# Kernel optimization log

Measured on AMD Instinct MI355X. Metric: run time of the kernel, lower is better.

## Reference

```python
import jax, jax.numpy as jnp
import numpy as np
import math

HAD_BLOCK = 1024


def fwht(x):
    """Fast Walsh-Hadamard transform along the last axis (size must be power of 2)."""
    orig_shape = x.shape
    n = orig_shape[-1]
    x = x.reshape(-1, n)
    h = 1
    while h < n:  # log2(n) stages; static Python loop, jit-friendly
        x = x.reshape(-1, n // (2 * h), 2, h)
        a = x[:, :, 0, :]
        b = x[:, :, 1, :]
        x = jnp.stack([a + b, a - b], axis=2).reshape(-1, n)
        h *= 2
    return x.reshape(orig_shape)


def setup_inputs() -> dict:
    key = jax.random.key(0)
    kx, kw = jax.random.split(key)
    B, S, D_in, D_out = 4, 4096, 4096, 4096
    x = jax.random.normal(kx, (B, S, D_in), dtype=jnp.float32)
    # nn.Parameter(weight / sqrt(had_block_size)) in __init__
    weight = jax.random.normal(kw, (D_out, D_in), dtype=jnp.float32) / math.sqrt(HAD_BLOCK)
    return {"x": x, "weight": weight}


def reference(x, weight):
    n = x.shape[-1]
    padded = ((n - 1) // HAD_BLOCK + 1) * HAD_BLOCK
    if padded != n:
        pad_width = [(0, 0)] * (x.ndim - 1) + [(0, padded - n)]
        x = jnp.pad(x, pad_width)
    mult = padded // HAD_BLOCK
    xb = x.reshape(x.shape[:-1] + (mult, HAD_BLOCK))
    xb = fwht(xb) * (1.0 / math.sqrt(HAD_BLOCK))
    xh = xb.reshape(x.shape[:-1] + (mult * HAD_BLOCK,))
    # F.linear: x @ weight.T
    return jnp.einsum('bsi,oi->bso', xh, weight)
```

## Files before the change

### kernel.cpp

```cpp
#include <hip/hip_runtime.h>
#include <hip/hip_bf16.h>
#include <stdint.h>


typedef __attribute__((ext_vector_type(8))) short    short8;
typedef __attribute__((ext_vector_type(4))) float    f32x4;
typedef __attribute__((ext_vector_type(8))) uint16_t u16x8;

static constexpr int MDIM = 16384;
static constexpr int NDIM = 4096;
static constexpr int KDIM = 4096;
static constexpr int BM = 256, BN = 256, BK = 64;
static constexpr int NT = KDIM / BK;

__device__ __forceinline__ uint16_t f2bf(float f) {
  union { float f; uint32_t u; } c; c.f = f;
  uint32_t u = c.u;
  return (uint16_t)((u + 0x7FFFu + ((u >> 16) & 1u)) >> 16);
}

__global__ __launch_bounds__(256) void cvt_x_kernel(const float* __restrict__ x,
                                                    uint16_t* __restrict__ xb, int n8) {
  int stride = gridDim.x * blockDim.x;
  for (int t = blockIdx.x * blockDim.x + threadIdx.x; t < n8; t += stride) {
    const float4* p = reinterpret_cast<const float4*>(x + (size_t)t * 8);
    float4 a = p[0], b = p[1];
    u16x8 o;
    o[0] = f2bf(a.x); o[1] = f2bf(a.y); o[2] = f2bf(a.z); o[3] = f2bf(a.w);
    o[4] = f2bf(b.x); o[5] = f2bf(b.y); o[6] = f2bf(b.z); o[7] = f2bf(b.w);
    *reinterpret_cast<u16x8*>(xb + (size_t)t * 8) = o;
  }
}

__global__ __launch_bounds__(256) void fwht_w_kernel(const float* __restrict__ W,
                                                     uint16_t* __restrict__ Wh) {
  __shared__ float s[1024];
  const int tid = threadIdx.x;
  const size_t base = (size_t)blockIdx.x * 1024;
  reinterpret_cast<float4*>(s)[tid] = reinterpret_cast<const float4*>(W + base)[tid];
  __syncthreads();
  for (int h = 1; h < 1024; h <<= 1) {
    #pragma unroll
    for (int pp = 0; pp < 2; ++pp) {
      int p = tid + pp * 256;
      int q = p & (h - 1);
      int i = ((p - q) << 1) | q;
      float a = s[i], b = s[i + h];
      s[i] = a + b;
      s[i + h] = a - b;
    }
    __syncthreads();
  }
  #pragma unroll
  for (int pp = 0; pp < 4; ++pp) {
    int i = tid + pp * 256;
    Wh[base + i] = f2bf(s[i] * 0.03125f);
  }
}


#define FENCE asm volatile("" ::: "memory")
#define SBAR  do { FENCE; __builtin_amdgcn_s_barrier(); \
                   __builtin_amdgcn_sched_barrier(0); } while (0)
#define LGKM0 do { asm volatile("s_waitcnt lgkmcnt(0)" ::: "memory"); \
                   __builtin_amdgcn_sched_barrier(0); } while (0)
#define VMC(n) do { asm volatile("s_waitcnt vmcnt(" #n ")" ::: "memory"); \
                    __builtin_amdgcn_sched_barrier(0); } while (0)

#define LDA4(DST, BUF, MLO, KOFF)                                              \
  do { _Pragma("unroll")                                                       \
    for (int m_ = 0; m_ < 4; ++m_)                                             \
      DST[m_] = *(const short8*)(aRd + (BUF)*32768 + ((MLO)+m_)*2048 + (KOFF)); \
  } while (0)

#define LDB4(DST, BUF, KOFF)                                                   \
  do { _Pragma("unroll")                                                       \
    for (int n_ = 0; n_ < 4; ++n_)                                             \
      DST[n_] = *(const short8*)(bRd + (BUF)*32768 + n_*2048 + (KOFF));        \
  } while (0)

#define MF16(AF, BF, MB)                                                       \
  do { __builtin_amdgcn_s_setprio(1);                                          \
    _Pragma("unroll")                                                          \
    for (int m_ = 0; m_ < 4; ++m_)                                             \
      _Pragma("unroll")                                                        \
      for (int n_ = 0; n_ < 4; ++n_)                                           \
        acc[(MB)+m_][n_] = __builtin_amdgcn_mfma_f32_16x16x32_bf16(            \
            AF[m_], BF[n_], acc[(MB)+m_][n_], 0, 0, 0);                        \
    __builtin_amdgcn_s_setprio(0);                                             \
  } while (0)

#define ITER(T1, T2, T3, FIN)                                                  \
  do {                                                                         \
    short8 aL[4], aH[4], bK[4];                                                \
     SBAR;                                                            \
    LDB4(bK, 0, k0off); LDA4(aL, 0, 0, k0off);                                 \
    stageAg(1, 1, (T1));                                                       \
    LGKM0; MF16(aL, bK, 0);                                                    \
     SBAR;                                                            \
    LDA4(aH, 0, 4, k0off);                                                     \
    stageB(1, 1, (T1));                                                        \
    LGKM0; MF16(aH, bK, 4);                                                    \
     SBAR;                                                            \
    LDB4(bK, 0, k1off); LDA4(aL, 0, 0, k1off);                                 \
    LGKM0; MF16(aL, bK, 0);                                                    \
     SBAR;                                                            \
    LDA4(aH, 0, 4, k1off);                                                     \
    if (!(FIN)) { stageB(0, 0, (T2)); stageAg(0, 0, (T2)); }                   \
    LGKM0; MF16(aH, bK, 4);                                                    \
    if (FIN) { VMC(0); } else { VMC(4); }                                      \
     SBAR;                                                            \
    LDB4(bK, 1, k0off); LDA4(aL, 1, 0, k0off);                                 \
    if (!(FIN)) stageAg(0, 1, (T2));                                           \
    LGKM0; MF16(aL, bK, 0);                                                    \
     SBAR;                                                            \
    LDA4(aH, 1, 4, k0off);                                                     \
    if (!(FIN)) stageB(0, 1, (T2));                                            \
    LGKM0; MF16(aH, bK, 4);                                                    \
     SBAR;                                                            \
    LDB4(bK, 1, k1off); LDA4(aL, 1, 0, k1off);                                 \
    LGKM0; MF16(aL, bK, 0);                                                    \
     SBAR;                                                            \
    LDA4(aH, 1, 4, k1off);                                                     \
    if (!(FIN)) { stageB(1, 0, (T3)); stageAg(1, 0, (T3)); }                   \
    LGKM0; MF16(aH, bK, 4);                                                    \
    if (!(FIN)) { VMC(4); }                                                    \
  } while (0)

__global__ __launch_bounds__(512, 2) void gemm_bt(const uint16_t* __restrict__ A,
                                                  const uint16_t* __restrict__ B,
                                                  float* __restrict__ C) {
  __shared__ __align__(16) uint16_t Ab[2][BM * BK];
  __shared__ __align__(16) uint16_t Bb[2][BN * BK];

  const int tid = threadIdx.x;
  const int wv  = tid >> 6;
  const int l   = tid & 63;

  const int xcd = blockIdx.x & 7;
  const int r_  = blockIdx.x >> 3;
  const int tm  = xcd * 8 + ((r_ & 31) >> 2);
  const int tn  = (r_ >> 5) * 4 + (r_ & 3);
  const int wm  = wv >> 2;
  const int wn  = wv & 3;

  const int t8  = tid >> 3;
  const int swz = (tid & 7) ^ ((tid >> 4) & 7);
  const uint16_t* sA = A + (size_t)(tm * BM + t8) * KDIM + swz * 8;
  const uint16_t* sB = B + (size_t)(tn * BN + t8) * KDIM + swz * 8;

  auto stageAg = [&](int buf, int g, int tk) {
    #pragma unroll
    for (int j = 0; j < 2; ++j)
      __builtin_amdgcn_global_load_lds(
          (const __attribute__((address_space(1))) unsigned int*)
              (sA + (size_t)(g * 64 + j * 128) * KDIM + tk * BK),
          (__attribute__((address_space(3))) unsigned int*)
              ((char*)&Ab[buf][0] + g * 8192 + j * 16384 + wv * 1024),
          16, 0, 0);
  };
  auto stageB = [&](int buf, int half, int tk) {
    #pragma unroll
    for (int j = 0; j < 2; ++j)
      __builtin_amdgcn_global_load_lds(
          (const __attribute__((address_space(1))) unsigned int*)
              (sB + (size_t)(half * 128 + j * 64) * KDIM + tk * BK),
          (__attribute__((address_space(3))) unsigned int*)
              ((char*)&Bb[buf][0] + half * 16384 + j * 8192 + wv * 1024),
          16, 0, 0);
  };

  const int lA = l & 15, hi = l >> 4;
  const int xr = (lA >> 1) & 7;
  const int k0off = (hi ^ xr) * 16;
  const int k1off = k0off ^ 64;
  const char* aRd = (const char*)&Ab[0][0] + (wm * 128 + lA) * 128;
  const char* bRd = (const char*)&Bb[0][0] + (wn * 64 + lA) * 128;

  f32x4 acc[8][4] = {};

  stageAg(0, 0, 0); stageAg(0, 1, 0); stageB(0, 0, 0); stageB(0, 1, 0);
  stageB(1, 0, 1);  stageAg(1, 0, 1);
  VMC(4);

  #pragma unroll 1
  for (int i = 0; i < NT / 2 - 1; ++i)
    ITER(2 * i + 1, 2 * i + 2, 2 * i + 3, 0);
  ITER(NT - 1, 0, 0, 1);

  float* Cp = C + (size_t)(tm * BM + wm * 128) * NDIM + tn * BN + wn * 64;
  const int co = hi * 4;
  #pragma unroll
  for (int m = 0; m < 8; ++m)
    #pragma unroll
    for (int n = 0; n < 4; ++n)
      #pragma unroll
      for (int j = 0; j < 4; ++j)
        Cp[(size_t)(m * 16 + co + j) * NDIM + n * 16 + lA] = acc[m][n][j];
}

extern "C" void kernel_launch(void* const* d_in, const int* in_sizes, int n_in,
                              void* d_out, int out_size, void* d_ws, size_t ws_size,
                              hipStream_t stream) {
  (void)in_sizes; (void)n_in; (void)out_size; (void)ws_size;
  const float* x = (const float*)d_in[0];
  const float* w = (const float*)d_in[1];
  float* out = (float*)d_out;

  uint16_t* xb = (uint16_t*)d_ws;
  uint16_t* wh = xb + (size_t)MDIM * KDIM;

  cvt_x_kernel<<<2048, 256, 0, stream>>>(x, xb, (int)((MDIM * (size_t)KDIM) / 8));
  fwht_w_kernel<<<(NDIM * KDIM) / 1024, 256, 0, stream>>>(w, wh);
  gemm_bt<<<(MDIM / BM) * (NDIM / BN), 512, 0, stream>>>(xb, wh, out);
}
```

Baseline: 604.9 us.

## Prefetch LDS fragments one phase ahead and drop explicit lgkmcnt waits

The GEMM main loop is restructured so that each phase issues the LDS reads for the next MFMA group before running the current one. This is a register-level software pipeline, using a second B-fragment buffer (bKa/bKb) and loading aL and aH together. The hard `s_waitcnt lgkmcnt(0)` before every MFMA block is replaced with a plain scheduling barrier, leaving the compiler to insert finer-grained waits. The aim is to hide LDS read latency behind matrix math, at the cost of more fragment registers and a tighter dependence on the compiler placing waits correctly around barriers and buffer reuse.

After: 638.6 us. 1.06x slower.

```diff
diff --git a/kernel.cpp b/kernel.cpp
--- a/kernel.cpp
+++ b/kernel.cpp
@@ -62,8 +62,7 @@
 #define FENCE asm volatile("" ::: "memory")
 #define SBAR  do { FENCE; __builtin_amdgcn_s_barrier(); \
                    __builtin_amdgcn_sched_barrier(0); } while (0)
-#define LGKM0 do { asm volatile("s_waitcnt lgkmcnt(0)" ::: "memory"); \
-                   __builtin_amdgcn_sched_barrier(0); } while (0)
+#define SCHED0 __builtin_amdgcn_sched_barrier(0)
 #define VMC(n) do { asm volatile("s_waitcnt vmcnt(" #n ")" ::: "memory"); \
                     __builtin_amdgcn_sched_barrier(0); } while (0)
 
@@ -92,38 +91,36 @@
 
 #define ITER(T1, T2, T3, FIN)                                                  \
   do {                                                                         \
-    short8 aL[4], aH[4], bK[4];                                                \
-     SBAR;                                                            \
-    LDB4(bK, 0, k0off); LDA4(aL, 0, 0, k0off);                                 \
+    short8 aL[4], aH[4], bKa[4], bKb[4];                                       \
+     SBAR;                                                            \
     stageAg(1, 1, (T1));                                                       \
-    LGKM0; MF16(aL, bK, 0);                                                    \
-     SBAR;                                                            \
-    LDA4(aH, 0, 4, k0off);                                                     \
+    LDB4(bKa, 0, k0off); LDA4(aL, 0, 0, k0off); LDA4(aH, 0, 4, k0off);         \
+    SCHED0; MF16(aL, bKa, 0);                                                  \
+     SBAR;                                                            \
     stageB(1, 1, (T1));                                                        \
-    LGKM0; MF16(aH, bK, 4);                                                    \
-     SBAR;                                                            \
-    LDB4(bK, 0, k1off); LDA4(aL, 0, 0, k1off);                                 \
-    LGKM0; MF16(aL, bK, 0);                                                    \
+    LDB4(bKb, 0, k1off); LDA4(aL, 0, 0, k1off);                                \
+    SCHED0; MF16(aH, bKa, 4);                                                  \
      SBAR;                                                            \
     LDA4(aH, 0, 4, k1off);                                                     \
+    SCHED0; MF16(aL, bKb, 0);                                                  \
+     SBAR;                                                            \
     if (!(FIN)) { stageB(0, 0, (T2)); stageAg(0, 0, (T2)); }                   \
-    LGKM0; MF16(aH, bK, 4);                                                    \
+    SCHED0; MF16(aH, bKb, 4);                                                  \
     if (FIN) { VMC(0); } else { VMC(4); }                                      \
      SBAR;                                                            \
-    LDB4(bK, 1, k0off); LDA4(aL, 1, 0, k0off);                                 \
     if (!(FIN)) stageAg(0, 1, (T2));                                           \
-    LGKM0; MF16(aL, bK, 0);                                                    \
-     SBAR;                                                            \
-    LDA4(aH, 1, 4, k0off);                                                     \
+    LDB4(bKa, 1, k0off); LDA4(aL, 1, 0, k0off); LDA4(aH, 1, 4, k0off);         \
+    SCHED0; MF16(aL, bKa, 0);                                                  \
+     SBAR;                                                            \
     if (!(FIN)) stageB(0, 1, (T2));                                            \
-    LGKM0; MF16(aH, bK, 4);                                                    \
-     SBAR;                                                            \
-    LDB4(bK, 1, k1off); LDA4(aL, 1, 0, k1off);                                 \
-    LGKM0; MF16(aL, bK, 0);                                                    \
+    LDB4(bKb, 1, k1off); LDA4(aL, 1, 0, k1off);                                \
+    SCHED0; MF16(aH, bKa, 4);                                                  \
      SBAR;                                                            \
     LDA4(aH, 1, 4, k1off);                                                     \
+    SCHED0; MF16(aL, bKb, 0);                                                  \
+     SBAR;                                                            \
     if (!(FIN)) { stageB(1, 0, (T3)); stageAg(1, 0, (T3)); }                   \
-    LGKM0; MF16(aH, bK, 4);                                                    \
+    SCHED0; MF16(aH, bKb, 4);                                                  \
     if (!(FIN)) { VMC(4); }                                                    \
   } while (0)
 
```
